# Performance work log

Hardware: AMD Instinct MI355X
Metric: run time of the kernel (lower is better)

Reference implementation:

```python
import jax, jax.numpy as jnp
import numpy as np
import math

V, D, H, L, MLP = 32000, 1024, 16, 4, 4
B, T = 2, 1024
HD = D // H
ALIBI_BIAS_MAX = 8.0
EPS = 1e-5


def _ln(x, g, b):
    m = jnp.mean(x, -1, keepdims=True)
    v = jnp.mean((x - m) ** 2, -1, keepdims=True)
    return (x - m) * jax.lax.rsqrt(v + EPS) * g + b


def setup_inputs() -> dict:
    key = jax.random.key(0)
    ks = jax.random.split(key, 12)
    s = 0.02
    inp = {
        "input_ids": jax.random.randint(ks[0], (B, T), 0, V),
        "wte": jax.random.normal(ks[1], (V, D), jnp.float32) * s,
        "ln1_g": jnp.ones((L, D), jnp.float32),
        "ln1_b": jnp.zeros((L, D), jnp.float32),
        "attn_w": jax.random.normal(ks[2], (L, 3 * D, D), jnp.float32) * s,
        "attn_b": jnp.zeros((L, 3 * D), jnp.float32),
        "proj_w": jax.random.normal(ks[3], (L, D, D), jnp.float32) * s,
        "proj_b": jnp.zeros((L, D), jnp.float32),
        "ln2_g": jnp.ones((L, D), jnp.float32),
        "ln2_b": jnp.zeros((L, D), jnp.float32),
        "fc_w": jax.random.normal(ks[4], (L, MLP * D, D), jnp.float32) * s,
        "fc_b": jnp.zeros((L, MLP * D), jnp.float32),
        "fc2_w": jax.random.normal(ks[5], (L, D, MLP * D), jnp.float32) * s,
        "fc2_b": jnp.zeros((L, D), jnp.float32),
        "lnf_g": jnp.ones((D,), jnp.float32),
        "lnf_b": jnp.zeros((D,), jnp.float32),
        "lm_head_w": jax.random.normal(ks[6], (V, D), jnp.float32) * s,
    }
    return inp


def reference(input_ids, wte, ln1_g, ln1_b, attn_w, attn_b, proj_w, proj_b,
              ln2_g, ln2_b, fc_w, fc_b, fc2_w, fc2_b, lnf_g, lnf_b, lm_head_w):
    b, t = input_ids.shape
    x = wte[input_ids]  # [B,T,D]

    # causal + ALiBi bias, [H,T,T]
    pos = jnp.arange(t)
    rel = -jnp.abs(pos[None, :] - pos[:, None]).astype(jnp.float32)  # -|i-j|
    m = jnp.arange(1, H + 1, dtype=jnp.float32) * (ALIBI_BIAS_MAX / H)
    alibi = rel[None, :, :] * (2.0 ** (-m))[:, None, None]
    causal = jnp.where(pos[None, :] > pos[:, None], -jnp.inf, 0.0)
    bias = alibi + causal[None]
    scale = 1.0 / math.sqrt(HD)

    def block(x, p):
        l1g, l1b, aw, ab, pw, pb, l2g, l2b, fw, fb, f2w, f2b = p
        h = _ln(x, l1g, l1b)
        qkv = h @ aw.T + ab  # [B,T,3D]
        q, k, v = jnp.split(qkv, 3, axis=-1)
        q = q.reshape(b, t, H, HD).transpose(0, 2, 1, 3)
        k = k.reshape(b, t, H, HD).transpose(0, 2, 1, 3)
        v = v.reshape(b, t, H, HD).transpose(0, 2, 1, 3)
        att = jnp.einsum('bhid,bhjd->bhij', q, k) * scale + bias[None]
        att = jax.nn.softmax(att, axis=-1)
        y = jnp.einsum('bhij,bhjd->bhid', att, v)
        y = y.transpose(0, 2, 1, 3).reshape(b, t, D)
        x = x + (y @ pw.T + pb)
        h2 = _ln(x, l2g, l2b)
        x = x + (jax.nn.gelu(h2 @ fw.T + fb, approximate=False) @ f2w.T + f2b)
        return x, None

    x, _ = jax.lax.scan(
        block, x,
        (ln1_g, ln1_b, attn_w, attn_b, proj_w, proj_b,
         ln2_g, ln2_b, fc_w, fc_b, fc2_w, fc2_b))
    x = _ln(x, lnf_g, lnf_b)
    logits = x @ lm_head_w.T  # [B,T,V]
    return logits
```

## Files before the change

kernel.cpp:

```cpp
#include <hip/hip_runtime.h>
#include <hip/hip_bf16.h>
#include <math.h>

typedef __hip_bfloat16 bf16;
typedef __attribute__((ext_vector_type(4))) float f32x4;
typedef __attribute__((ext_vector_type(8))) short short8;

constexpr int Bc = 2, Tc = 1024, Dc = 1024, Hc = 16, Lc = 4, MLPc = 4096, Vc = 32000, HDc = 64;

__device__ __forceinline__ unsigned short f2bu(float f) {
    __hip_bfloat16 h = __float2bfloat16(f);
    unsigned short u;
    __builtin_memcpy(&u, &h, 2);
    return u;
}
__device__ __forceinline__ float bu2f(unsigned short u) {
    __hip_bfloat16 h;
    __builtin_memcpy(&h, &u, 2);
    return __bfloat162float(h);
}

__device__ __forceinline__ void gl2lds16(const bf16* g, bf16* l) {
    __builtin_amdgcn_global_load_lds(
        (const __attribute__((address_space(1))) void*)g,
        (__attribute__((address_space(3))) void*)l, 16, 0, 0);
}

enum { EPI_BIAS_BF16 = 0, EPI_GELU = 1, EPI_RESADD = 2, EPI_F32 = 3, EPI_QKV = 4 };

template <int EPI>
__device__ __forceinline__ void epi_store(float v, int row, int col, void* Cv,
                                          int ldc, const float* bias) {
    if constexpr (EPI == EPI_BIAS_BF16) {
        v += bias[col];
        ((bf16*)Cv)[(size_t)row * ldc + col] = __float2bfloat16(v);
    } else if constexpr (EPI == EPI_GELU) {
        v += bias[col];
        v = 0.5f * v * (1.0f + erff(v * 0.70710678118f));
        ((bf16*)Cv)[(size_t)row * ldc + col] = __float2bfloat16(v);
    } else if constexpr (EPI == EPI_RESADD) {
        bf16* C = (bf16*)Cv;
        size_t idx = (size_t)row * ldc + col;
        float xo = __bfloat162float(C[idx]);
        C[idx] = __float2bfloat16(xo + v + bias[col]);
    } else if constexpr (EPI == EPI_F32) {
        ((float*)Cv)[(size_t)row * ldc + col] = v;
    } else if constexpr (EPI == EPI_QKV) {
        v += bias[col];
        bf16 bv = __float2bfloat16(v);
        int b = row >> 10, t = row & 1023;
        int seg = col >> 10;
        int cc = col & 1023;
        int h = cc >> 6, hd = cc & 63;
        bf16* base = (bf16*)Cv;
        base[(size_t)seg * 2097152 + ((size_t)(b * Hc + h) * Tc + t) * HDc + hd] = bv;
    }
}

template <int MH, int KK>
__device__ __forceinline__ void load_a4(short8 (&af)[4], const char* Abase,
                                        int wm, int lr, int lq) {
#pragma unroll
    for (int fi = 0; fi < 4; fi++) {
        int r = MH * 128 + wm * 64 + fi * 16 + lr;
        int cb = (KK * 64 + lq * 16) ^ ((r & 7) << 4);
        af[fi] = *reinterpret_cast<const short8*>(Abase + (size_t)r * 128 + cb);
    }
}
template <int NH, int KK>
__device__ __forceinline__ void load_b2(short8 (&bf2)[2], const char* Bbase,
                                        int wn, int lr, int lq) {
#pragma unroll
    for (int fj = 0; fj < 2; fj++) {
        int r = NH * 128 + wn * 32 + fj * 16 + lr;
        int cb = (KK * 64 + lq * 16) ^ ((r & 7) << 4);
        bf2[fj] = *reinterpret_cast<const short8*>(Bbase + (size_t)r * 128 + cb);
    }
}
template <int MH, int NH>
__device__ __forceinline__ void mma8(f32x4 (&acc)[2][2][4][2],
                                     const short8 (&af)[4], const short8 (&bf2)[2]) {
#pragma unroll
    for (int fi = 0; fi < 4; fi++)
#pragma unroll
        for (int fj = 0; fj < 2; fj++)
            acc[MH][NH][fi][fj] = __builtin_amdgcn_mfma_f32_16x16x32_bf16(
                af[fi], bf2[fj], acc[MH][NH][fi][fj], 0, 0, 0);
}

template <int EPI>
__global__ __launch_bounds__(512) void gemm_8p(
    const bf16* __restrict__ A, int lda,
    const bf16* __restrict__ Bm, int ldb,
    void* __restrict__ Cv, int ldc,
    const float* __restrict__ bias, int K)
{
    constexpr int BM = 256, BN = 256, BK = 64;
    __shared__ alignas(16) bf16 As[2][BM][BK];
    __shared__ alignas(16) bf16 Bs[2][BN][BK];

    const int tid = threadIdx.x;
    const int lane = tid & 63;
    const int w = tid >> 6;
    const int wm = w >> 2;
    const int wn = w & 3;

    int nwg = gridDim.x * gridDim.y;
    int orig = blockIdx.y * gridDim.x + blockIdx.x;
    int q = nwg >> 3, rr = nwg & 7, xcd = orig & 7, lid = orig >> 3;
    int wg = (xcd < rr ? xcd * (q + 1) : rr * (q + 1) + (xcd - rr) * q) + lid;
    int im = wg % gridDim.x;
    int in = wg / gridDim.x;

    const bf16* Ab = A + (size_t)im * BM * lda;
    const bf16* Bb = Bm + (size_t)in * BN * ldb;

    const int sr = lane >> 3;
    const int scs = ((lane & 7) ^ sr) * 8;
    const int lr = lane & 15, lq = lane >> 4;

    f32x4 acc[2][2][4][2];
#pragma unroll
    for (int a = 0; a < 2; a++)
#pragma unroll
        for (int b = 0; b < 2; b++)
#pragma unroll
            for (int c = 0; c < 4; c++)
#pragma unroll
                for (int d = 0; d < 2; d++) acc[a][b][c][d] = (f32x4){0.f, 0.f, 0.f, 0.f};

    const int NT = K / BK;

    auto stage_half = [&](int buf, int sg, int k0) {
        const bool isB = (sg == 1 || sg == 2);
        const bf16* gp = isB ? Bb : Ab;
        const int ld = isB ? ldb : lda;
        bf16* ls = isB ? &Bs[buf][0][0] : &As[buf][0][0];
        const int half = (sg == 2 || sg == 3) ? 1 : 0;
#pragma unroll
        for (int i = 0; i < 2; i++) {
            int r0 = half * 128 + i * 64 + w * 8;
            gl2lds16(gp + (size_t)(r0 + sr) * ld + k0 + scs, ls + r0 * BK);
        }
    };

    stage_half(0, 0, 0);
    stage_half(0, 1, 0);
    stage_half(0, 2, 0);
    stage_half(0, 3, 0);
    stage_half(1, 0, BK);
    stage_half(1, 1, BK);
    asm volatile("s_waitcnt vmcnt(6)" ::: "memory");
    __builtin_amdgcn_s_barrier();
    asm volatile("" ::: "memory");

    short8 af[4], b0k0[2], b0k1[2], b1k0[2], b1k1[2];

    for (int t = 0; t < NT; t++) {
        const int cur = t & 1;
        const char* Abase = (const char*)&As[cur][0][0];
        const char* Bbase = (const char*)&Bs[cur][0][0];
        const bool pf1 = (t + 1 < NT);
        const bool pf2 = (t + 2 < NT);
        const int kn1 = (t + 1) * BK;
        const int kn2 = (t + 2) * BK;
        const bool tail = (t >= NT - 2);

        load_a4<0, 0>(af, Abase, wm, lr, lq);
        load_b2<0, 0>(b0k0, Bbase, wn, lr, lq);
        load_b2<1, 0>(b1k0, Bbase, wn, lr, lq);
        if (pf1) stage_half(cur ^ 1, 2, kn1);
        asm volatile("s_waitcnt lgkmcnt(0)" ::: "memory");
        __builtin_amdgcn_s_barrier();
        __builtin_amdgcn_s_setprio(1);
        mma8<0, 0>(acc, af, b0k0);
        mma8<0, 1>(acc, af, b1k0);
        __builtin_amdgcn_s_setprio(0);

        load_a4<0, 1>(af, Abase, wm, lr, lq);
        load_b2<0, 1>(b0k1, Bbase, wn, lr, lq);
        load_b2<1, 1>(b1k1, Bbase, wn, lr, lq);
        if (pf1) stage_half(cur ^ 1, 3, kn1);
        asm volatile("s_waitcnt lgkmcnt(0)" ::: "memory");
        if (tail) asm volatile("s_waitcnt vmcnt(0)" ::: "memory");
        else      asm volatile("s_waitcnt vmcnt(8)" ::: "memory");
        __builtin_amdgcn_s_barrier();
        __builtin_amdgcn_s_setprio(1);
        mma8<0, 0>(acc, af, b0k1);
        mma8<0, 1>(acc, af, b1k1);
        __builtin_amdgcn_s_setprio(0);

        load_a4<1, 0>(af, Abase, wm, lr, lq);
        if (pf2) stage_half(cur, 0, kn2);
        asm volatile("s_waitcnt lgkmcnt(0)" ::: "memory");
        __builtin_amdgcn_s_barrier();
        __builtin_amdgcn_s_setprio(1);
        mma8<1, 0>(acc, af, b0k0);
        mma8<1, 1>(acc, af, b1k0);
        __builtin_amdgcn_s_setprio(0);

        load_a4<1, 1>(af, Abase, wm, lr, lq);
        if (pf2) stage_half(cur, 1, kn2);
        asm volatile("s_waitcnt lgkmcnt(0)" ::: "memory");
        if (tail) asm volatile("s_waitcnt vmcnt(0)" ::: "memory");
        else      asm volatile("s_waitcnt vmcnt(6)" ::: "memory");
        __builtin_amdgcn_s_barrier();
        __builtin_amdgcn_s_setprio(1);
        mma8<1, 0>(acc, af, b0k1);
        mma8<1, 1>(acc, af, b1k1);
        __builtin_amdgcn_s_setprio(0);
        asm volatile("" ::: "memory");
    }

#pragma unroll
    for (int mh = 0; mh < 2; mh++)
#pragma unroll
        for (int nh = 0; nh < 2; nh++)
#pragma unroll
            for (int fi = 0; fi < 4; fi++)
#pragma unroll
                for (int fj = 0; fj < 2; fj++)
#pragma unroll
                    for (int r = 0; r < 4; r++) {
                        int row = im * 256 + mh * 128 + wm * 64 + fi * 16 + lq * 4 + r;
                        int col = in * 256 + nh * 128 + wn * 32 + fj * 16 + lr;
                        epi_store<EPI>(acc[mh][nh][fi][fj][r], row, col, Cv, ldc, bias);
                    }
}

template <int BM, int BN, int BK, int EPI, bool SWZG>
__global__ __launch_bounds__(256) void gemm_fast(
    const bf16* __restrict__ A, int lda,
    const bf16* __restrict__ Bm, int ldb,
    void* __restrict__ Cv, int ldc,
    const float* __restrict__ bias, int K)
{
    static_assert(BK == 64, "staging geometry assumes BK=64");
    __shared__ alignas(16) bf16 As[2][BM][BK];
    __shared__ alignas(16) bf16 Bs[2][BN][BK];

    const int tid = threadIdx.x;
    const int lane = tid & 63;
    const int w = tid >> 6;
    const int wm = w >> 1, wn = w & 1;
    constexpr int WM = BM / 2, WN = BN / 2;
    constexpr int FM = WM / 16, FN = WN / 16;
    constexpr int RPI = 512 / BK;
    constexpr int AI = BM / (4 * RPI);
    constexpr int BI = BN / (4 * RPI);

    int im, in;
    if constexpr (SWZG) {
        int nwg = gridDim.x * gridDim.y;
        int orig = blockIdx.y * gridDim.x + blockIdx.x;
        int q = nwg >> 3, rr = nwg & 7, xcd = orig & 7, lid = orig >> 3;
        int wg = (xcd < rr ? xcd * (q + 1) : rr * (q + 1) + (xcd - rr) * q) + lid;
        im = wg % gridDim.x;
        in = wg / gridDim.x;
    } else {
        im = blockIdx.y;
        in = blockIdx.x;
    }

    const bf16* Ab = A + (size_t)im * BM * lda;
    const bf16* Bb = Bm + (size_t)in * BN * ldb;

    const int sr = lane >> 3;
    const int scs = (((lane & 7) ^ sr) * 8);
    const int lr = lane & 15, lq = lane >> 4;

    f32x4 acc[FM][FN];
#pragma unroll
    for (int i = 0; i < FM; i++)
#pragma unroll
        for (int j = 0; j < FN; j++) acc[i][j] = (f32x4){0.f, 0.f, 0.f, 0.f};

    auto stage = [&](int buf, int k0) {
#pragma unroll
        for (int i = 0; i < AI; i++) {
            int row = (w * AI + i) * RPI;
            gl2lds16(Ab + (size_t)(row + sr) * lda + k0 + scs, &As[buf][row][0]);
        }
#pragma unroll
        for (int i = 0; i < BI; i++) {
            int row = (w * BI + i) * RPI;
            gl2lds16(Bb + (size_t)(row + sr) * ldb + k0 + scs, &Bs[buf][row][0]);
        }
    };

    const int NT = K / BK;
    stage(0, 0);
    __syncthreads();

    for (int t = 0; t < NT; t++) {
        const int cur = t & 1;
        if (t + 1 < NT) stage(cur ^ 1, (t + 1) * BK);

        const char* Abase = (const char*)&As[cur][0][0];
        const char* Bbase = (const char*)&Bs[cur][0][0];
#pragma unroll
        for (int kk = 0; kk < BK / 32; kk++) {
            short8 af[FM], bfr[FN];
#pragma unroll
            for (int i = 0; i < FM; i++) {
                int r = wm * WM + i * 16 + lr;
                int cb = (kk * 64 + lq * 16) ^ ((r & 7) << 4);
                af[i] = *reinterpret_cast<const short8*>(Abase + (size_t)r * (BK * 2) + cb);
            }
#pragma unroll
            for (int j = 0; j < FN; j++) {
                int r = wn * WN + j * 16 + lr;
                int cb = (kk * 64 + lq * 16) ^ ((r & 7) << 4);
                bfr[j] = *reinterpret_cast<const short8*>(Bbase + (size_t)r * (BK * 2) + cb);
            }
#pragma unroll
            for (int i = 0; i < FM; i++)
#pragma unroll
                for (int j = 0; j < FN; j++)
                    acc[i][j] = __builtin_amdgcn_mfma_f32_16x16x32_bf16(af[i], bfr[j], acc[i][j], 0, 0, 0);
        }
        __syncthreads();
    }

#pragma unroll
    for (int i = 0; i < FM; i++)
#pragma unroll
        for (int j = 0; j < FN; j++)
#pragma unroll
            for (int r = 0; r < 4; r++) {
                int row = im * BM + wm * WM + i * 16 + lq * 4 + r;
                int col = in * BN + wn * WN + j * 16 + lr;
                epi_store<EPI>(acc[i][j][r], row, col, Cv, ldc, bias);
            }
}

template <int BM, int BN, int BK, int EPI>
__global__ __launch_bounds__(256) void gemm_bt_f32(
    const bf16* __restrict__ A, int lda,
    const float* __restrict__ Bm, int ldb,
    void* __restrict__ Cv, int ldc,
    const float* __restrict__ bias, int K)
{
    constexpr int BKP = BK + 8;
    __shared__ bf16 As[BM][BKP];
    __shared__ bf16 Bs[BN][BKP];
    const int tid = threadIdx.x;
    const int lane = tid & 63;
    const int w = tid >> 6;
    const int wm = w >> 1, wn = w & 1;
    constexpr int WM = BM / 2, WN = BN / 2;
    constexpr int FM = WM / 16, FN = WN / 16;
    const int bx = blockIdx.x, by = blockIdx.y;
    const bf16* Ab = A + (size_t)by * BM * lda;
    const float* Bb = Bm + (size_t)bx * BN * ldb;
    f32x4 acc[FM][FN];
#pragma unroll
    for (int i = 0; i < FM; i++)
#pragma unroll
        for (int j = 0; j < FN; j++) acc[i][j] = (f32x4){0.f, 0.f, 0.f, 0.f};
    const int lr = lane & 15, lq = lane >> 4;
    for (int k0 = 0; k0 < K; k0 += BK) {
        constexpr int AC = (BM * BK) / (256 * 8);
#pragma unroll
        for (int i = 0; i < AC; i++) {
            int c = tid + i * 256;
            int row = c / (BK / 8);
            int kc = (c % (BK / 8)) * 8;
            *reinterpret_cast<int4*>(&As[row][kc]) =
                *reinterpret_cast<const int4*>(Ab + (size_t)row * lda + k0 + kc);
        }
        constexpr int BC = (BN * BK) / (256 * 4);
#pragma unroll
        for (int i = 0; i < BC; i++) {
            int c = tid + i * 256;
            int row = c / (BK / 4);
            int kc = (c % (BK / 4)) * 4;
            float4 v = *reinterpret_cast<const float4*>(Bb + (size_t)row * ldb + k0 + kc);
            unsigned long long p = (unsigned long long)f2bu(v.x) |
                                   ((unsigned long long)f2bu(v.y) << 16) |
                                   ((unsigned long long)f2bu(v.z) << 32) |
                                   ((unsigned long long)f2bu(v.w) << 48);
            *reinterpret_cast<unsigned long long*>(&Bs[row][kc]) = p;
        }
        __syncthreads();
#pragma unroll
        for (int kk = 0; kk < BK / 32; kk++) {
            short8 af[FM], bfr[FN];
#pragma unroll
            for (int i = 0; i < FM; i++)
                af[i] = *reinterpret_cast<const short8*>(&As[wm * WM + i * 16 + lr][kk * 32 + lq * 8]);
#pragma unroll
            for (int j = 0; j < FN; j++)
                bfr[j] = *reinterpret_cast<const short8*>(&Bs[wn * WN + j * 16 + lr][kk * 32 + lq * 8]);
#pragma unroll
            for (int i = 0; i < FM; i++)
#pragma unroll
                for (int j = 0; j < FN; j++)
                    acc[i][j] = __builtin_amdgcn_mfma_f32_16x16x32_bf16(af[i], bfr[j], acc[i][j], 0, 0, 0);
        }
        __syncthreads();
    }
#pragma unroll
    for (int i = 0; i < FM; i++)
#pragma unroll
        for (int j = 0; j < FN; j++)
#pragma unroll
            for (int r = 0; r < 4; r++) {
                int row = by * BM + wm * WM + i * 16 + lq * 4 + r;
                int col = bx * BN + wn * WN + j * 16 + lr;
                epi_store<EPI>(acc[i][j][r], row, col, Cv, ldc, bias);
            }
}

__global__ __launch_bounds__(256) void flash_attn(
    const bf16* __restrict__ q, const bf16* __restrict__ kbuf,
    const bf16* __restrict__ vt, bf16* __restrict__ y)
{
    __shared__ alignas(16) bf16 Ks[128 * 64];
    __shared__ alignas(16) bf16 Vs[64 * 128];
    __shared__ alignas(16) bf16 Ps[4 * 16 * 136];

    const int tid = threadIdx.x;
    const int lane = tid & 63;
    const int w = tid >> 6;
    const int lr = lane & 15, lq = lane >> 4;
    const int qi = (int)gridDim.x - 1 - (int)blockIdx.x;
    const int z = blockIdx.y;
    const int b = z >> 4, h = z & 15;
    const float slope = exp2f(-0.5f * (float)(h + 1));

    const bf16* qz = q + (size_t)z * (Tc * HDc);
    const bf16* kz = kbuf + (size_t)z * (Tc * HDc);
    const bf16* vz = vt + (size_t)z * (HDc * Tc);

    const int rowbase = qi * 64 + w * 16;

    short8 qf[2];
#pragma unroll
    for (int kk = 0; kk < 2; kk++)
        qf[kk] = *reinterpret_cast<const short8*>(
            qz + (size_t)(rowbase + lr) * HDc + kk * 32 + lq * 8);

    float m_old[4], l_sum[4];
#pragma unroll
    for (int r = 0; r < 4; r++) { m_old[r] = -3.0e38f; l_sum[r] = 0.f; }
    f32x4 o[4];
#pragma unroll
    for (int dj = 0; dj < 4; dj++) o[dj] = (f32x4){0.f, 0.f, 0.f, 0.f};

    bf16* Pw = Ps + w * 16 * 136;

    const int nkv = (qi * 64 + 63) / 128 + 1;
    for (int kv = 0; kv < nkv; kv++) {
#pragma unroll
        for (int i = 0; i < 4; i++) {
            int rbase = w * 32 + i * 8;
            int row = rbase + (lane >> 3);
            int slot = lane & 7;
            gl2lds16(kz + (size_t)(kv * 128 + row) * HDc + ((slot ^ (row & 7)) * 8),
                     &Ks[rbase * 64]);
        }
#pragma unroll
        for (int i = 0; i < 4; i++) {
            int rbase = w * 16 + i * 4;
            int row = rbase + lq;
            gl2lds16(vz + (size_t)row * Tc + kv * 128 + ((lr ^ (row & 7)) * 8),
                     &Vs[rbase * 128]);
        }
        __syncthreads();

        f32x4 s[8];
#pragma unroll
        for (int j = 0; j < 8; j++) s[j] = (f32x4){0.f, 0.f, 0.f, 0.f};
#pragma unroll
        for (int kk = 0; kk < 2; kk++) {
#pragma unroll
            for (int j = 0; j < 8; j++) {
                int row = j * 16 + lr;
                int cb = ((kk * 4 + lq) ^ (row & 7)) << 4;
                short8 bfr = *reinterpret_cast<const short8*>(
                    (const char*)Ks + row * 128 + cb);
                s[j] = __builtin_amdgcn_mfma_f32_16x16x32_bf16(qf[kk], bfr, s[j], 0, 0, 0);
            }
        }

        float mt[4];
#pragma unroll
        for (int r = 0; r < 4; r++) mt[r] = -3.0e38f;
#pragma unroll
        for (int j = 0; j < 8; j++) {
            int col = kv * 128 + j * 16 + lr;
#pragma unroll
            for (int r = 0; r < 4; r++) {
                int rowg = rowbase + lq * 4 + r;
                float v = s[j][r] * 0.125f - (float)(rowg - col) * slope;
                v = (col > rowg) ? -3.0e38f : v;
                s[j][r] = v;
                mt[r] = fmaxf(mt[r], v);
            }
        }
#pragma unroll
        for (int r = 0; r < 4; r++)
#pragma unroll
            for (int off = 1; off < 16; off <<= 1)
                mt[r] = fmaxf(mt[r], __shfl_xor(mt[r], off));

        float f[4], rs[4];
#pragma unroll
        for (int r = 0; r < 4; r++) {
            float mn = fmaxf(m_old[r], mt[r]);
            f[r] = __expf(m_old[r] - mn);
            m_old[r] = mn;
            rs[r] = 0.f;
        }
#pragma unroll
        for (int j = 0; j < 8; j++)
#pragma unroll
            for (int r = 0; r < 4; r++) {
                float p = __expf(s[j][r] - m_old[r]);
                s[j][r] = p;
                rs[r] += p;
            }
#pragma unroll
        for (int r = 0; r < 4; r++) {
#pragma unroll
            for (int off = 1; off < 16; off <<= 1)
                rs[r] += __shfl_xor(rs[r], off);
            l_sum[r] = l_sum[r] * f[r] + rs[r];
        }

#pragma unroll
        for (int j = 0; j < 8; j++)
#pragma unroll
            for (int r = 0; r < 4; r++)
                Pw[(lq * 4 + r) * 136 + j * 16 + lr] = __float2bfloat16(s[j][r]);

#pragma unroll
        for (int dj = 0; dj < 4; dj++)
#pragma unroll
            for (int r = 0; r < 4; r++) o[dj][r] *= f[r];

        __syncthreads();

#pragma unroll
        for (int kk = 0; kk < 4; kk++) {
            short8 pa = *reinterpret_cast<const short8*>(
                (const char*)Pw + lr * 272 + kk * 64 + lq * 16);
#pragma unroll
            for (int dj = 0; dj < 4; dj++) {
                int row = dj * 16 + lr;
                int cb = ((kk * 4 + lq) ^ (row & 7)) << 4;
                short8 vb = *reinterpret_cast<const short8*>(
                    (const char*)Vs + row * 256 + cb);
                o[dj] = __builtin_amdgcn_mfma_f32_16x16x32_bf16(pa, vb, o[dj], 0, 0, 0);
            }
        }
        __syncthreads();
    }

#pragma unroll
    for (int dj = 0; dj < 4; dj++)
#pragma unroll
        for (int r = 0; r < 4; r++) {
            int rowg = rowbase + lq * 4 + r;
            float outv = o[dj][r] / l_sum[r];
            y[((size_t)b * Tc + rowg) * Dc + h * HDc + dj * 16 + lr] =
                __float2bfloat16(outv);
        }
}

__global__ __launch_bounds__(256) void f2b8(const float* __restrict__ in,
                                            bf16* __restrict__ out, long n) {
    long i = ((long)blockIdx.x * 256 + threadIdx.x) * 8;
    if (i >= n) return;
    float4 a = *reinterpret_cast<const float4*>(in + i);
    float4 b = *reinterpret_cast<const float4*>(in + i + 4);
    unsigned long long p0 = (unsigned long long)f2bu(a.x) |
                            ((unsigned long long)f2bu(a.y) << 16) |
                            ((unsigned long long)f2bu(a.z) << 32) |
                            ((unsigned long long)f2bu(a.w) << 48);
    unsigned long long p1 = (unsigned long long)f2bu(b.x) |
                            ((unsigned long long)f2bu(b.y) << 16) |
                            ((unsigned long long)f2bu(b.z) << 32) |
                            ((unsigned long long)f2bu(b.w) << 48);
    *reinterpret_cast<unsigned long long*>(out + i) = p0;
    *reinterpret_cast<unsigned long long*>(out + i + 4) = p1;
}

__global__ __launch_bounds__(256) void embed_kernel(const int* __restrict__ ids,
                                                    const float* __restrict__ wte,
                                                    bf16* __restrict__ x) {
    int row = blockIdx.x;
    int t = threadIdx.x;
    int id = ids[row];
    float4 v = reinterpret_cast<const float4*>(wte + (size_t)id * Dc)[t];
    unsigned long long p = (unsigned long long)f2bu(v.x) |
                           ((unsigned long long)f2bu(v.y) << 16) |
                           ((unsigned long long)f2bu(v.z) << 32) |
                           ((unsigned long long)f2bu(v.w) << 48);
    *reinterpret_cast<unsigned long long*>(x + (size_t)row * Dc + t * 4) = p;
}

__global__ __launch_bounds__(256) void ln_kernel(const bf16* __restrict__ x,
                                                 const float* __restrict__ g,
                                                 const float* __restrict__ b,
                                                 bf16* __restrict__ out) {
    int row = blockIdx.x;
    int t = threadIdx.x;
    unsigned long long uv = *reinterpret_cast<const unsigned long long*>(
        x + (size_t)row * Dc + t * 4);
    float vv[4];
#pragma unroll
    for (int j = 0; j < 4; j++) vv[j] = bu2f((unsigned short)(uv >> (16 * j)));
    float s = vv[0] + vv[1] + vv[2] + vv[3];
    float s2 = vv[0] * vv[0] + vv[1] * vv[1] + vv[2] * vv[2] + vv[3] * vv[3];
#pragma unroll
    for (int o = 32; o > 0; o >>= 1) {
        s += __shfl_down(s, o);
        s2 += __shfl_down(s2, o);
    }
    __shared__ float sm[8];
    int wid = t >> 6, ln = t & 63;
    if (ln == 0) { sm[wid] = s; sm[4 + wid] = s2; }
    __syncthreads();
    if (t == 0) {
        float ts = sm[0] + sm[1] + sm[2] + sm[3];
        float ts2 = sm[4] + sm[5] + sm[6] + sm[7];
        sm[0] = ts; sm[4] = ts2;
    }
    __syncthreads();
    float mean = sm[0] * (1.0f / Dc);
    float var = sm[4] * (1.0f / Dc) - mean * mean;
    float rstd = rsqrtf(var + 1e-5f);
    int c0 = t * 4;
    unsigned long long p = 0;
#pragma unroll
    for (int j = 0; j < 4; j++) {
        float val = (vv[j] - mean) * rstd * g[c0 + j] + b[c0 + j];
        p |= (unsigned long long)f2bu(val) << (16 * j);
    }
    *reinterpret_cast<unsigned long long*>(out + (size_t)row * Dc + c0) = p;
}

__global__ __launch_bounds__(256) void v2vt(const bf16* __restrict__ v,
                                            bf16* __restrict__ vt) {
    int idx = blockIdx.x * 256 + threadIdx.x;
    int tc = idx & 127;
    int t0 = tc * 8;
    int rest = idx >> 7;
    int hd = rest & 63;
    int z = rest >> 6;
    const bf16* src = v + ((size_t)z * Tc) * HDc + hd;
    unsigned long long p0 = 0, p1 = 0;
#pragma unroll
    for (int i = 0; i < 4; i++) {
        unsigned short u;
        __builtin_memcpy(&u, src + (size_t)(t0 + i) * HDc, 2);
        p0 |= (unsigned long long)u << (16 * i);
    }
#pragma unroll
    for (int i = 0; i < 4; i++) {
        unsigned short u;
        __builtin_memcpy(&u, src + (size_t)(t0 + 4 + i) * HDc, 2);
        p1 |= (unsigned long long)u << (16 * i);
    }
    bf16* dst = vt + ((size_t)z * HDc + hd) * Tc + t0;
    *reinterpret_cast<unsigned long long*>(dst) = p0;
    *reinterpret_cast<unsigned long long*>(dst + 4) = p1;
}

extern "C" void kernel_launch(void* const* d_in, const int* in_sizes, int n_in,
                              void* d_out, int out_size, void* d_ws, size_t ws_size,
                              hipStream_t stream) {
    const int* ids = (const int*)d_in[0];
    const float* wte = (const float*)d_in[1];
    const float* ln1g = (const float*)d_in[2];
    const float* ln1b = (const float*)d_in[3];
    const float* attw = (const float*)d_in[4];
    const float* attb = (const float*)d_in[5];
    const float* projw = (const float*)d_in[6];
    const float* projb = (const float*)d_in[7];
    const float* ln2g = (const float*)d_in[8];
    const float* ln2b = (const float*)d_in[9];
    const float* fcw = (const float*)d_in[10];
    const float* fcb = (const float*)d_in[11];
    const float* fc2w = (const float*)d_in[12];
    const float* fc2b = (const float*)d_in[13];
    const float* lnfg = (const float*)d_in[14];
    const float* lnfb = (const float*)d_in[15];
    const float* lmw = (const float*)d_in[16];

    const int M = Bc * Tc;
    char* ws = (char*)d_ws;
    size_t off = 0;
    auto carve = [&](size_t bytes) { char* p = ws + off; off += (bytes + 255) & ~(size_t)255; return p; };

    bf16* x = (bf16*)carve((size_t)M * Dc * 2);
    bf16* h = (bf16*)carve((size_t)M * Dc * 2);
    bf16* qkvb = (bf16*)carve((size_t)3 * 2097152 * 2);
    bf16* vt = (bf16*)carve((size_t)Bc * Hc * HDc * Tc * 2);
    bf16* y = (bf16*)carve((size_t)M * Dc * 2);
    bf16* mlp = (bf16*)carve((size_t)M * MLPc * 2);
    bf16* q = qkvb;
    bf16* kb = qkvb + 2097152;
    bf16* vtmp = qkvb + 4194304;

    const long nLM = (long)Vc * Dc;
    bool has_wlm = ws_size >= off + (size_t)nLM * 2;
    bf16* wlm = nullptr;
    if (has_wlm) wlm = (bf16*)carve((size_t)nLM * 2);

    const long nAW = (long)Lc * 3 * Dc * Dc;
    const long nPW = (long)Lc * Dc * Dc;
    const long nFW = (long)Lc * MLPc * Dc;
    const long nF2W = (long)Lc * Dc * MLPc;
    bf16* awAll = (bf16*)d_out;
    bf16* pwAll = awAll + nAW;
    bf16* fwAll = pwAll + nPW;
    bf16* f2wAll = fwAll + nFW;

    embed_kernel<<<M, 256, 0, stream>>>(ids, wte, x);

    f2b8<<<(int)(nAW / 8 / 256), 256, 0, stream>>>(attw, awAll, nAW);
    f2b8<<<(int)(nPW / 8 / 256), 256, 0, stream>>>(projw, pwAll, nPW);
    f2b8<<<(int)(nFW / 8 / 256), 256, 0, stream>>>(fcw, fwAll, nFW);
    f2b8<<<(int)(nF2W / 8 / 256), 256, 0, stream>>>(fc2w, f2wAll, nF2W);
    if (has_wlm)
        f2b8<<<(int)(nLM / 8 / 256), 256, 0, stream>>>(lmw, wlm, nLM);

    for (int l = 0; l < Lc; l++) {
        bf16* aw_b = awAll + (size_t)l * 3 * Dc * Dc;
        bf16* pw_b = pwAll + (size_t)l * Dc * Dc;
        bf16* fw_b = fwAll + (size_t)l * MLPc * Dc;
        bf16* f2w_b = f2wAll + (size_t)l * Dc * MLPc;

        ln_kernel<<<M, 256, 0, stream>>>(x, ln1g + l * Dc, ln1b + l * Dc, h);

        gemm_fast<128, 128, 64, EPI_QKV, true>
            <<<dim3(M / 128, 3 * Dc / 128, 1), 256, 0, stream>>>(
                h, Dc, aw_b, Dc, qkvb, 0, attb + l * 3 * Dc, Dc);

        v2vt<<<(Bc * Hc * HDc * (Tc / 8)) / 256, 256, 0, stream>>>(vtmp, vt);

        flash_attn<<<dim3(Tc / 64, Bc * Hc), 256, 0, stream>>>(q, kb, vt, y);

        gemm_fast<128, 64, 64, EPI_RESADD, true>
            <<<dim3(M / 128, Dc / 64, 1), 256, 0, stream>>>(
                y, Dc, pw_b, Dc, x, Dc, projb + l * Dc, Dc);

        ln_kernel<<<M, 256, 0, stream>>>(x, ln2g + l * Dc, ln2b + l * Dc, h);

        gemm_fast<128, 128, 64, EPI_GELU, true>
            <<<dim3(M / 128, MLPc / 128, 1), 256, 0, stream>>>(
                h, Dc, fw_b, Dc, mlp, MLPc, fcb + l * MLPc, Dc);

        gemm_fast<128, 64, 64, EPI_RESADD, true>
            <<<dim3(M / 128, Dc / 64, 1), 256, 0, stream>>>(
                mlp, MLPc, f2w_b, MLPc, x, Dc, fc2b + l * Dc, MLPc);
    }

    ln_kernel<<<M, 256, 0, stream>>>(x, lnfg, lnfb, h);

    if (has_wlm)
        gemm_8p<EPI_F32>
            <<<dim3(M / 256, Vc / 256, 1), 512, 0, stream>>>(
                h, Dc, wlm, Dc, (float*)d_out, Vc, nullptr, Dc);
    else
        gemm_bt_f32<128, 128, 64, EPI_F32>
            <<<dim3(Vc / 128, M / 128, 1), 256, 0, stream>>>(
                h, Dc, lmw, Dc, (float*)d_out, Vc, nullptr, Dc);
}
```

Measured before the change: 1.148 ms.

## Shrink GEMM K-tile to 32 for occupancy and double-buffer attention K/V loads

The GEMM kernel's K tile drops from 64 to 32, halving LDS use, with a new 4-slot XOR swizzle, adjusted vmcnt waits, and a launch-bounds hint for more resident workgroups. Its per-iteration schedule now reuses one B fragment set across M halves. The flash-attention kernel gets double-buffered K/V tiles so the next tile's global-to-LDS copy overlaps compute, and a block barrier becomes a per-wave LDS wait. The GEMM now has more iterations and barriers per K, and the changed vmcnt and barrier logic risks ordering hazards.

```diff
diff --git a/kernel.cpp b/kernel.cpp
--- a/kernel.cpp
+++ b/kernel.cpp
@@ -57,24 +57,24 @@
     }
 }
 
-template <int MH, int KK>
-__device__ __forceinline__ void load_a4(short8 (&af)[4], const char* Abase,
-                                        int wm, int lr, int lq) {
+template <int MH>
+__device__ __forceinline__ void load_a32(short8 (&af)[4], const char* Abase,
+                                         int wm, int lr, int lq) {
 #pragma unroll
     for (int fi = 0; fi < 4; fi++) {
         int r = MH * 128 + wm * 64 + fi * 16 + lr;
-        int cb = (KK * 64 + lq * 16) ^ ((r & 7) << 4);
-        af[fi] = *reinterpret_cast<const short8*>(Abase + (size_t)r * 128 + cb);
-    }
-}
-template <int NH, int KK>
-__device__ __forceinline__ void load_b2(short8 (&bf2)[2], const char* Bbase,
-                                        int wn, int lr, int lq) {
+        int cb = (lq ^ (r & 3)) << 4;
+        af[fi] = *reinterpret_cast<const short8*>(Abase + (size_t)r * 64 + cb);
+    }
+}
+template <int NH>
+__device__ __forceinline__ void load_b32(short8 (&bf2)[2], const char* Bbase,
+                                         int wn, int lr, int lq) {
 #pragma unroll
     for (int fj = 0; fj < 2; fj++) {
         int r = NH * 128 + wn * 32 + fj * 16 + lr;
-        int cb = (KK * 64 + lq * 16) ^ ((r & 7) << 4);
-        bf2[fj] = *reinterpret_cast<const short8*>(Bbase + (size_t)r * 128 + cb);
+        int cb = (lq ^ (r & 3)) << 4;
+        bf2[fj] = *reinterpret_cast<const short8*>(Bbase + (size_t)r * 64 + cb);
     }
 }
 template <int MH, int NH>
@@ -89,13 +89,13 @@
 }
 
 template <int EPI>
-__global__ __launch_bounds__(512) void gemm_8p(
+__global__ __launch_bounds__(512, 4) void gemm_8p(
     const bf16* __restrict__ A, int lda,
     const bf16* __restrict__ Bm, int ldb,
     void* __restrict__ Cv, int ldc,
     const float* __restrict__ bias, int K)
 {
-    constexpr int BM = 256, BN = 256, BK = 64;
+    constexpr int BM = 256, BN = 256, BK = 32;
     __shared__ alignas(16) bf16 As[2][BM][BK];
     __shared__ alignas(16) bf16 Bs[2][BN][BK];
 
@@ -115,8 +115,8 @@
     const bf16* Ab = A + (size_t)im * BM * lda;
     const bf16* Bb = Bm + (size_t)in * BN * ldb;
 
-    const int sr = lane >> 3;
-    const int scs = ((lane & 7) ^ sr) * 8;
+    const int srr = lane >> 2;
+    const int scs = ((lane & 3) ^ (srr & 3)) * 8;
     const int lr = lane & 15, lq = lane >> 4;
 
     f32x4 acc[2][2][4][2];
@@ -137,11 +137,8 @@
         const int ld = isB ? ldb : lda;
         bf16* ls = isB ? &Bs[buf][0][0] : &As[buf][0][0];
         const int half = (sg == 2 || sg == 3) ? 1 : 0;
-#pragma unroll
-        for (int i = 0; i < 2; i++) {
-            int r0 = half * 128 + i * 64 + w * 8;
-            gl2lds16(gp + (size_t)(r0 + sr) * ld + k0 + scs, ls + r0 * BK);
-        }
+        int r0 = half * 128 + w * 16;
+        gl2lds16(gp + (size_t)(r0 + srr) * ld + k0 + scs, ls + r0 * BK);
     };
 
     stage_half(0, 0, 0);
@@ -150,11 +147,11 @@
     stage_half(0, 3, 0);
     stage_half(1, 0, BK);
     stage_half(1, 1, BK);
-    asm volatile("s_waitcnt vmcnt(6)" ::: "memory");
+    asm volatile("s_waitcnt vmcnt(4)" ::: "memory");
     __builtin_amdgcn_s_barrier();
     asm volatile("" ::: "memory");
 
-    short8 af[4], b0k0[2], b0k1[2], b1k0[2], b1k1[2];
+    short8 af[4], b0[2], b1[2];
 
     for (int t = 0; t < NT; t++) {
         const int cur = t & 1;
@@ -164,50 +161,43 @@
         const bool pf2 = (t + 2 < NT);
         const int kn1 = (t + 1) * BK;
         const int kn2 = (t + 2) * BK;
-        const bool tail = (t >= NT - 2);
-
-        load_a4<0, 0>(af, Abase, wm, lr, lq);
-        load_b2<0, 0>(b0k0, Bbase, wn, lr, lq);
-        load_b2<1, 0>(b1k0, Bbase, wn, lr, lq);
+        const bool tail = (t >= NT - 3);
+
+        load_a32<0>(af, Abase, wm, lr, lq);
+        load_b32<0>(b0, Bbase, wn, lr, lq);
         if (pf1) stage_half(cur ^ 1, 2, kn1);
         asm volatile("s_waitcnt lgkmcnt(0)" ::: "memory");
+        if (tail) asm volatile("s_waitcnt vmcnt(0)" ::: "memory");
+        else      asm volatile("s_waitcnt vmcnt(4)" ::: "memory");
         __builtin_amdgcn_s_barrier();
         __builtin_amdgcn_s_setprio(1);
-        mma8<0, 0>(acc, af, b0k0);
-        mma8<0, 1>(acc, af, b1k0);
+        mma8<0, 0>(acc, af, b0);
         __builtin_amdgcn_s_setprio(0);
 
-        load_a4<0, 1>(af, Abase, wm, lr, lq);
-        load_b2<0, 1>(b0k1, Bbase, wn, lr, lq);
-        load_b2<1, 1>(b1k1, Bbase, wn, lr, lq);
+        load_b32<1>(b1, Bbase, wn, lr, lq);
         if (pf1) stage_half(cur ^ 1, 3, kn1);
         asm volatile("s_waitcnt lgkmcnt(0)" ::: "memory");
         if (tail) asm volatile("s_waitcnt vmcnt(0)" ::: "memory");
-        else      asm volatile("s_waitcnt vmcnt(8)" ::: "memory");
+        else      asm volatile("s_waitcnt vmcnt(4)" ::: "memory");
         __builtin_amdgcn_s_barrier();
         __builtin_amdgcn_s_setprio(1);
-        mma8<0, 0>(acc, af, b0k1);
-        mma8<0, 1>(acc, af, b1k1);
+        mma8<0, 1>(acc, af, b1);
         __builtin_amdgcn_s_setprio(0);
 
-        load_a4<1, 0>(af, Abase, wm, lr, lq);
+        load_a32<1>(af, Abase, wm, lr, lq);
         if (pf2) stage_half(cur, 0, kn2);
         asm volatile("s_waitcnt lgkmcnt(0)" ::: "memory");
         __builtin_amdgcn_s_barrier();
         __builtin_amdgcn_s_setprio(1);
-        mma8<1, 0>(acc, af, b0k0);
-        mma8<1, 1>(acc, af, b1k0);
+        mma8<1, 1>(acc, af, b1);
         __builtin_amdgcn_s_setprio(0);
 
-        load_a4<1, 1>(af, Abase, wm, lr, lq);
         if (pf2) stage_half(cur, 1, kn2);
-        asm volatile("s_waitcnt lgkmcnt(0)" ::: "memory");
         if (tail) asm volatile("s_waitcnt vmcnt(0)" ::: "memory");
-        else      asm volatile("s_waitcnt vmcnt(6)" ::: "memory");
+        else      asm volatile("s_waitcnt vmcnt(4)" ::: "memory");
         __builtin_amdgcn_s_barrier();
         __builtin_amdgcn_s_setprio(1);
-        mma8<1, 0>(acc, af, b0k1);
-        mma8<1, 1>(acc, af, b1k1);
+        mma8<1, 0>(acc, af, b0);
         __builtin_amdgcn_s_setprio(0);
         asm volatile("" ::: "memory");
     }
@@ -416,8 +406,8 @@
     const bf16* __restrict__ q, const bf16* __restrict__ kbuf,
     const bf16* __restrict__ vt, bf16* __restrict__ y)
 {
-    __shared__ alignas(16) bf16 Ks[128 * 64];
-    __shared__ alignas(16) bf16 Vs[64 * 128];
+    __shared__ alignas(16) bf16 Ks[2][128 * 64];
+    __shared__ alignas(16) bf16 Vs[2][64 * 128];
     __shared__ alignas(16) bf16 Ps[4 * 16 * 136];
 
     const int tid = threadIdx.x;
@@ -450,24 +440,40 @@
 
     bf16* Pw = Ps + w * 16 * 136;
 
-    const int nkv = (qi * 64 + 63) / 128 + 1;
-    for (int kv = 0; kv < nkv; kv++) {
+    auto stage_kv = [&](int kv, int buf) {
 #pragma unroll
         for (int i = 0; i < 4; i++) {
             int rbase = w * 32 + i * 8;
             int row = rbase + (lane >> 3);
             int slot = lane & 7;
             gl2lds16(kz + (size_t)(kv * 128 + row) * HDc + ((slot ^ (row & 7)) * 8),
-                     &Ks[rbase * 64]);
+                     &Ks[buf][rbase * 64]);
         }
 #pragma unroll
         for (int i = 0; i < 4; i++) {
             int rbase = w * 16 + i * 4;
             int row = rbase + lq;
             gl2lds16(vz + (size_t)row * Tc + kv * 128 + ((lr ^ (row & 7)) * 8),
-                     &Vs[rbase * 128]);
-        }
-        __syncthreads();
+                     &Vs[buf][rbase * 128]);
+        }
+    };
+
+    const int nkv = (qi * 64 + 63) / 128 + 1;
+    stage_kv(0, 0);
+
+    for (int kv = 0; kv < nkv; kv++) {
+        const int cur = kv & 1;
+        if (kv + 1 < nkv) {
+            stage_kv(kv + 1, cur ^ 1);
+            asm volatile("s_waitcnt vmcnt(8)" ::: "memory");
+        } else {
+            asm volatile("s_waitcnt vmcnt(0)" ::: "memory");
+        }
+        __builtin_amdgcn_s_barrier();
+        asm volatile("" ::: "memory");
+
+        const char* Kb = (const char*)&Ks[cur][0];
+        const char* Vb = (const char*)&Vs[cur][0];
 
         f32x4 s[8];
 #pragma unroll
@@ -478,8 +484,7 @@
             for (int j = 0; j < 8; j++) {
                 int row = j * 16 + lr;
                 int cb = ((kk * 4 + lq) ^ (row & 7)) << 4;
-                short8 bfr = *reinterpret_cast<const short8*>(
-                    (const char*)Ks + row * 128 + cb);
+                short8 bfr = *reinterpret_cast<const short8*>(Kb + row * 128 + cb);
                 s[j] = __builtin_amdgcn_mfma_f32_16x16x32_bf16(qf[kk], bfr, s[j], 0, 0, 0);
             }
         }
@@ -540,7 +545,7 @@
 #pragma unroll
             for (int r = 0; r < 4; r++) o[dj][r] *= f[r];
 
-        __syncthreads();
+        asm volatile("s_waitcnt lgkmcnt(0)" ::: "memory");
 
 #pragma unroll
         for (int kk = 0; kk < 4; kk++) {
@@ -550,12 +555,13 @@
             for (int dj = 0; dj < 4; dj++) {
                 int row = dj * 16 + lr;
                 int cb = ((kk * 4 + lq) ^ (row & 7)) << 4;
-                short8 vb = *reinterpret_cast<const short8*>(
-                    (const char*)Vs + row * 256 + cb);
+                short8 vb = *reinterpret_cast<const short8*>(Vb + row * 256 + cb);
                 o[dj] = __builtin_amdgcn_mfma_f32_16x16x32_bf16(pa, vb, o[dj], 0, 0, 0);
             }
         }
-        __syncthreads();
+        asm volatile("s_waitcnt lgkmcnt(0)" ::: "memory");
+        __builtin_amdgcn_s_barrier();
+        asm volatile("" ::: "memory");
     }
 
 #pragma unroll
```

After: 2.023 ms. +76.3%, slower.

## Double-buffer K/V tiles in flash attention to overlap loads with compute

Applied to the files above, without the earlier changes.

Gives the flash attention kernel two LDS buffers for K and V. The next KV tile is issued with global_load_lds before the current tile is computed, and a partial vmcnt wait lets those loads overlap with the MFMA work. The mid-iteration __syncthreads is replaced by a wave-local lgkmcnt wait, since each wave's P tile is private to it. This doubles K/V LDS use, which may lower occupancy, and relies on hand-counted vmcnt values being correct.

```diff
diff --git a/kernel.cpp b/kernel.cpp
--- a/kernel.cpp
+++ b/kernel.cpp
@@ -416,8 +416,8 @@
     const bf16* __restrict__ q, const bf16* __restrict__ kbuf,
     const bf16* __restrict__ vt, bf16* __restrict__ y)
 {
-    __shared__ alignas(16) bf16 Ks[128 * 64];
-    __shared__ alignas(16) bf16 Vs[64 * 128];
+    __shared__ alignas(16) bf16 Ks[2][128 * 64];
+    __shared__ alignas(16) bf16 Vs[2][64 * 128];
     __shared__ alignas(16) bf16 Ps[4 * 16 * 136];
 
     const int tid = threadIdx.x;
@@ -450,24 +450,40 @@
 
     bf16* Pw = Ps + w * 16 * 136;
 
-    const int nkv = (qi * 64 + 63) / 128 + 1;
-    for (int kv = 0; kv < nkv; kv++) {
+    auto stage_kv = [&](int kv, int buf) {
 #pragma unroll
         for (int i = 0; i < 4; i++) {
             int rbase = w * 32 + i * 8;
             int row = rbase + (lane >> 3);
             int slot = lane & 7;
             gl2lds16(kz + (size_t)(kv * 128 + row) * HDc + ((slot ^ (row & 7)) * 8),
-                     &Ks[rbase * 64]);
+                     &Ks[buf][rbase * 64]);
         }
 #pragma unroll
         for (int i = 0; i < 4; i++) {
             int rbase = w * 16 + i * 4;
             int row = rbase + lq;
             gl2lds16(vz + (size_t)row * Tc + kv * 128 + ((lr ^ (row & 7)) * 8),
-                     &Vs[rbase * 128]);
-        }
-        __syncthreads();
+                     &Vs[buf][rbase * 128]);
+        }
+    };
+
+    const int nkv = (qi * 64 + 63) / 128 + 1;
+    stage_kv(0, 0);
+
+    for (int kv = 0; kv < nkv; kv++) {
+        const int cur = kv & 1;
+        if (kv + 1 < nkv) {
+            stage_kv(kv + 1, cur ^ 1);
+            asm volatile("s_waitcnt vmcnt(8)" ::: "memory");
+        } else {
+            asm volatile("s_waitcnt vmcnt(0)" ::: "memory");
+        }
+        __builtin_amdgcn_s_barrier();
+        asm volatile("" ::: "memory");
+
+        const char* Kb = (const char*)&Ks[cur][0];
+        const char* Vb = (const char*)&Vs[cur][0];
 
         f32x4 s[8];
 #pragma unroll
@@ -478,8 +494,7 @@
             for (int j = 0; j < 8; j++) {
                 int row = j * 16 + lr;
                 int cb = ((kk * 4 + lq) ^ (row & 7)) << 4;
-                short8 bfr = *reinterpret_cast<const short8*>(
-                    (const char*)Ks + row * 128 + cb);
+                short8 bfr = *reinterpret_cast<const short8*>(Kb + row * 128 + cb);
                 s[j] = __builtin_amdgcn_mfma_f32_16x16x32_bf16(qf[kk], bfr, s[j], 0, 0, 0);
             }
         }
@@ -540,7 +555,7 @@
 #pragma unroll
             for (int r = 0; r < 4; r++) o[dj][r] *= f[r];
 
-        __syncthreads();
+        asm volatile("s_waitcnt lgkmcnt(0)" ::: "memory");
 
 #pragma unroll
         for (int kk = 0; kk < 4; kk++) {
@@ -550,12 +565,13 @@
             for (int dj = 0; dj < 4; dj++) {
                 int row = dj * 16 + lr;
                 int cb = ((kk * 4 + lq) ^ (row & 7)) << 4;
-                short8 vb = *reinterpret_cast<const short8*>(
-                    (const char*)Vs + row * 256 + cb);
+                short8 vb = *reinterpret_cast<const short8*>(Vb + row * 256 + cb);
                 o[dj] = __builtin_amdgcn_mfma_f32_16x16x32_bf16(pa, vb, o[dj], 0, 0, 0);
             }
         }
-        __syncthreads();
+        asm volatile("s_waitcnt lgkmcnt(0)" ::: "memory");
+        __builtin_amdgcn_s_barrier();
+        asm volatile("" ::: "memory");
     }
 
 #pragma unroll
```

Result: slower. 1.190 ms (+3.7%).
